# Kernel tuning notes

Hardware: AMD Instinct MI355X
Metric: run time of the kernel (lower is better)

The kernel has to match this reference:

```python
import jax, jax.numpy as jnp
import numpy as np

N = 100000   # nodes
E = 1600000  # edges
D = 128      # in_dim == hidden_dim
EL = 100000  # label edges for decode


def setup_inputs() -> dict:
    key = jax.random.key(0)
    k1, k2, k3, k4, k5 = jax.random.split(key, 5)
    x = jax.random.normal(k1, (N, D), dtype=jnp.float32)
    edge_index = jax.random.randint(k2, (2, E), 0, N, dtype=jnp.int64)
    edge_label_index = jax.random.randint(k3, (2, EL), 0, N, dtype=jnp.int64)
    # Glorot-ish init for GCN weights
    scale = 1.0 / np.sqrt(D)
    W1 = jax.random.normal(k4, (D, D), dtype=jnp.float32) * scale
    W2 = jax.random.normal(k5, (D, D), dtype=jnp.float32) * scale
    b1 = jnp.zeros((D,), dtype=jnp.float32)
    b2 = jnp.zeros((D,), dtype=jnp.float32)
    return {"x": x, "edge_index": edge_index, "edge_label_index": edge_label_index,
            "W1": W1, "b1": b1, "W2": W2, "b2": b2}


def gcn_conv(x, src, dst, W, b, num_nodes):
    # PyG GCNConv: add self-loops, symmetric D^-1/2 A D^-1/2 normalization
    loop = jnp.arange(num_nodes, dtype=src.dtype)
    s = jnp.concatenate([src, loop])
    d = jnp.concatenate([dst, loop])
    deg = jax.ops.segment_sum(jnp.ones(d.shape, dtype=x.dtype), d, num_segments=num_nodes)
    dinv = jnp.where(deg > 0, jax.lax.rsqrt(jnp.maximum(deg, 1.0)), 0.0)
    norm = dinv[s] * dinv[d]                      # [E+N]
    h = x @ W                                     # [N, H]
    msg = h[s] * norm[:, None]                    # gather + scale
    out = jax.ops.segment_sum(msg, d, num_segments=num_nodes)  # scatter-add
    return out + b


def reference(x, edge_index, edge_label_index, W1, b1, W2, b2):
    src, dst = edge_index[0], edge_index[1]
    z = jax.nn.relu(gcn_conv(x, src, dst, W1, b1, N))
    z = jax.nn.relu(gcn_conv(z, src, dst, W2, b2, N))
    # decode: edge-wise dot product
    s, d = edge_label_index[0], edge_label_index[1]
    return jnp.sum(z[s] * z[d], axis=-1)          # [EL]
```

## Files before the change

### kernel.cpp

```cpp
#include <hip/hip_runtime.h>
#include <hip/hip_bf16.h>
#include <hip/hip_fp16.h>


typedef _Float16 half8 __attribute__((ext_vector_type(8)));
typedef float floatx4 __attribute__((ext_vector_type(4)));

#define BK_SHIFT 8
#define BSC_EDGES 2048
#define SLAB_CAP 5120
#define WPAD 136

__global__ __launch_bounds__(128) void k_wprep(const float* __restrict__ W1,
                                               const float* __restrict__ W2,
                                               _Float16* __restrict__ WT1,
                                               _Float16* __restrict__ WT2,
                                               int* __restrict__ bfill) {
    int b = blockIdx.x;
    const float* W = (b < 128) ? W1 : W2;
    _Float16* WT = (b < 128) ? WT1 : WT2;
    int k = b & 127;
    int c = threadIdx.x;
    WT[c * 128 + k] = (_Float16)W[k * 128 + c];
    if (b < 4) bfill[b * 128 + c] = 0;
}

__global__ __launch_bounds__(256) void k_bscatter(const int* __restrict__ src,
                                                  const int* __restrict__ dst,
                                                  int* __restrict__ bfill,
                                                  int2* __restrict__ pairs,
                                                  int E, int nbk) {
    __shared__ int lcnt[1024];
    __shared__ int delta[1024];
    __shared__ int ssum[256];
    __shared__ int2 stage[BSC_EDGES];
    int tid = threadIdx.x;
    int e0 = blockIdx.x * BSC_EDGES;
    int nloc = E - e0; if (nloc > BSC_EDGES) nloc = BSC_EDGES;

    for (int b = tid; b < nbk; b += 256) lcnt[b] = 0;
    __syncthreads();

    int d[BSC_EDGES / 256], s[BSC_EDGES / 256];
#pragma unroll
    for (int k = 0; k < BSC_EDGES / 256; ++k) {
        int e = e0 + k * 256 + tid;
        if (e < E) {
            d[k] = dst[e];
            s[k] = src[e];
            atomicAdd(&lcnt[d[k] >> BK_SHIFT], 1);
        } else d[k] = -1;
    }
    __syncthreads();

    const int gpb = (nbk + 255) >> 8;
    int c[4], mysum = 0;
    for (int t = 0; t < gpb; ++t) {
        int b = tid * gpb + t;
        c[t] = (b < nbk) ? lcnt[b] : 0;
        mysum += c[t];
    }
    ssum[tid] = mysum;
    __syncthreads();
    for (int off = 1; off < 256; off <<= 1) {
        int t = (tid >= off) ? ssum[tid - off] : 0;
        __syncthreads();
        ssum[tid] += t;
        __syncthreads();
    }
    int base = ssum[tid] - mysum;
    for (int t = 0; t < gpb; ++t) {
        int b = tid * gpb + t;
        if (b < nbk) {
            int g = c[t] ? atomicAdd(&bfill[b], c[t]) : 0;
            delta[b] = b * SLAB_CAP + g - base;
            lcnt[b] = base;
            base += c[t];
        }
    }
    __syncthreads();

#pragma unroll
    for (int k = 0; k < BSC_EDGES / 256; ++k) {
        if (d[k] >= 0) {
            int b = d[k] >> BK_SHIFT;
            int lp = atomicAdd(&lcnt[b], 1);
            int2 p; p.x = s[k]; p.y = d[k];
            stage[lp] = p;
        }
    }
    __syncthreads();

    for (int j = tid; j < nloc; j += 256) {
        int2 p = stage[j];
        pairs[delta[p.y >> BK_SHIFT] + j] = p;
    }
}

template <typename AT>
__global__ __launch_bounds__(256) void k_csr_gemm(const int2* __restrict__ pairs,
                                                  const int* __restrict__ bfill,
                                                  int* __restrict__ row_start,
                                                  int* __restrict__ cnt,
                                                  float* __restrict__ dinv,
                                                  int* __restrict__ srcs,
                                                  const AT* __restrict__ X,
                                                  const _Float16* __restrict__ WT,
                                                  _Float16* __restrict__ G,
                                                  int n, int nbk) {
    __shared__ __align__(16) char smem[128 * WPAD * 2];
    int tid = threadIdx.x;

    if ((int)blockIdx.x < nbk) {
        int* lcnt = (int*)smem;
        int* lpos = lcnt + 256;
        int b = blockIdx.x;
        lcnt[tid] = 0;
        __syncthreads();
        int beg = b * SLAB_CAP, end = beg + bfill[b];
        for (int i = beg + tid; i < end; i += 256)
            atomicAdd(&lcnt[pairs[i].y & 255], 1);
        __syncthreads();
        int c = lcnt[tid];
        lpos[tid] = c;
        __syncthreads();
        for (int off = 1; off < 256; off <<= 1) {
            int t = (tid >= off) ? lpos[tid - off] : 0;
            __syncthreads();
            lpos[tid] += t;
            __syncthreads();
        }
        int rs = beg + lpos[tid] - c;
        int v = (b << BK_SHIFT) + tid;
        if (v < n) {
            row_start[v] = rs;
            cnt[v] = c;
            dinv[v] = rsqrtf((float)c + 1.0f);
        }
        __syncthreads();
        lpos[tid] = rs;
        __syncthreads();
        for (int i = beg + tid; i < end; i += 256) {
            int2 p = pairs[i];
            int loc = atomicAdd(&lpos[p.y & 255], 1);
            srcs[loc] = p.x;
        }
        return;
    }

    _Float16* Wl = (_Float16*)smem;
    {
        const half8* w8 = (const half8*)WT;
#pragma unroll
        for (int i = 0; i < 8; ++i) {
            int idx = i * 256 + tid;
            int r = idx >> 4, cc = idx & 15;
            *(half8*)(Wl + r * WPAD + cc * 8) = w8[idx];
        }
    }
    __syncthreads();

    auto loadA = [](const AT* p) -> half8 {
        if constexpr (sizeof(AT) == 4) {
            const float4* f = (const float4*)p;
            float4 f0 = f[0], f1 = f[1];
            half8 a;
            a[0] = (_Float16)f0.x; a[1] = (_Float16)f0.y;
            a[2] = (_Float16)f0.z; a[3] = (_Float16)f0.w;
            a[4] = (_Float16)f1.x; a[5] = (_Float16)f1.y;
            a[6] = (_Float16)f1.z; a[7] = (_Float16)f1.w;
            return a;
        } else {
            return *(const half8*)p;
        }
    };

    int bid = blockIdx.x - nbk;
    int wave = tid >> 6, lane = tid & 63;
    int q = lane >> 4, ln = lane & 15;
    int m0 = bid * 128 + wave * 32;
    int mA0 = m0 + ln;      if (mA0 >= n) mA0 = n - 1;
    int mA1 = m0 + 16 + ln; if (mA1 >= n) mA1 = n - 1;
    const AT* xr0 = X + (size_t)mA0 * 128;
    const AT* xr1 = X + (size_t)mA1 * 128;

    floatx4 acc[2][8];
#pragma unroll
    for (int p = 0; p < 2; ++p)
#pragma unroll
        for (int t = 0; t < 8; ++t) acc[p][t] = (floatx4){0.f, 0.f, 0.f, 0.f};

#pragma unroll
    for (int kc = 0; kc < 128; kc += 32) {
        half8 a0 = loadA(xr0 + kc + q * 8);
        half8 a1 = loadA(xr1 + kc + q * 8);
#pragma unroll
        for (int t = 0; t < 8; ++t) {
            half8 b = *(const half8*)(Wl + (size_t)(t * 16 + ln) * WPAD + kc + q * 8);
            acc[0][t] = __builtin_amdgcn_mfma_f32_16x16x32_f16(a0, b, acc[0][t], 0, 0, 0);
            acc[1][t] = __builtin_amdgcn_mfma_f32_16x16x32_f16(a1, b, acc[1][t], 0, 0, 0);
        }
    }

#pragma unroll
    for (int p = 0; p < 2; ++p) {
#pragma unroll
        for (int r = 0; r < 4; ++r) {
            int row = m0 + p * 16 + q * 4 + r;
            if (row < n) {
                _Float16* grow = G + (size_t)row * 128 + ln;
#pragma unroll
                for (int t = 0; t < 8; ++t)
                    grow[t * 16] = (_Float16)acc[p][t][r];
            }
        }
    }
}

template <typename AT>
__global__ __launch_bounds__(256) void k_gemm_mfma(const AT* __restrict__ X,
                                                   const _Float16* __restrict__ WT,
                                                   _Float16* __restrict__ G, int n) {
    __shared__ _Float16 Wl[128 * WPAD];
    int tid = threadIdx.x;
    {
        const half8* w8 = (const half8*)WT;
#pragma unroll
        for (int i = 0; i < 8; ++i) {
            int idx = i * 256 + tid;
            int r = idx >> 4, cc = idx & 15;
            *(half8*)(Wl + r * WPAD + cc * 8) = w8[idx];
        }
    }
    __syncthreads();

    auto loadA = [](const AT* p) -> half8 {
        if constexpr (sizeof(AT) == 4) {
            const float4* f = (const float4*)p;
            float4 f0 = f[0], f1 = f[1];
            half8 a;
            a[0] = (_Float16)f0.x; a[1] = (_Float16)f0.y;
            a[2] = (_Float16)f0.z; a[3] = (_Float16)f0.w;
            a[4] = (_Float16)f1.x; a[5] = (_Float16)f1.y;
            a[6] = (_Float16)f1.z; a[7] = (_Float16)f1.w;
            return a;
        } else {
            return *(const half8*)p;
        }
    };

    int wave = tid >> 6, lane = tid & 63;
    int q = lane >> 4, ln = lane & 15;
    int m0 = blockIdx.x * 128 + wave * 32;
    int mA0 = m0 + ln;      if (mA0 >= n) mA0 = n - 1;
    int mA1 = m0 + 16 + ln; if (mA1 >= n) mA1 = n - 1;
    const AT* xr0 = X + (size_t)mA0 * 128;
    const AT* xr1 = X + (size_t)mA1 * 128;

    floatx4 acc[2][8];
#pragma unroll
    for (int p = 0; p < 2; ++p)
#pragma unroll
        for (int t = 0; t < 8; ++t) acc[p][t] = (floatx4){0.f, 0.f, 0.f, 0.f};

#pragma unroll
    for (int kc = 0; kc < 128; kc += 32) {
        half8 a0 = loadA(xr0 + kc + q * 8);
        half8 a1 = loadA(xr1 + kc + q * 8);
#pragma unroll
        for (int t = 0; t < 8; ++t) {
            half8 b = *(const half8*)(Wl + (size_t)(t * 16 + ln) * WPAD + kc + q * 8);
            acc[0][t] = __builtin_amdgcn_mfma_f32_16x16x32_f16(a0, b, acc[0][t], 0, 0, 0);
            acc[1][t] = __builtin_amdgcn_mfma_f32_16x16x32_f16(a1, b, acc[1][t], 0, 0, 0);
        }
    }

#pragma unroll
    for (int p = 0; p < 2; ++p) {
#pragma unroll
        for (int r = 0; r < 4; ++r) {
            int row = m0 + p * 16 + q * 4 + r;
            if (row < n) {
                _Float16* grow = G + (size_t)row * 128 + ln;
#pragma unroll
                for (int t = 0; t < 8; ++t)
                    grow[t * 16] = (_Float16)acc[p][t][r];
            }
        }
    }
}

__global__ __launch_bounds__(256) void k_gather_relu(const _Float16* __restrict__ G,
                                                     const int* __restrict__ srcs,
                                                     const int* __restrict__ row_start,
                                                     const int* __restrict__ cnt,
                                                     const float* __restrict__ dinv,
                                                     const float* __restrict__ bias,
                                                     _Float16* __restrict__ Z, int n) {
    int v = blockIdx.x * 16 + (threadIdx.x >> 4);
    int lane = threadIdx.x & 15;
    if (v >= n) return;
    const half8* G8 = (const half8*)G;

    float dv = dinv[v];
    half8 self = G8[(size_t)v * 16 + lane];
    float acc[8], acc2[8];
#pragma unroll
    for (int j = 0; j < 8; ++j) { acc[j] = dv * (float)self[j]; acc2[j] = 0.f; }

    int beg = row_start[v], deg = cnt[v];
    int e = 0;
    for (; e + 3 < deg; e += 4) {
        int s0 = srcs[beg + e];
        int s1 = srcs[beg + e + 1];
        int s2 = srcs[beg + e + 2];
        int s3 = srcs[beg + e + 3];
        float d0 = dinv[s0];
        float d1 = dinv[s1];
        float d2 = dinv[s2];
        float d3 = dinv[s3];
        half8 t0 = G8[(size_t)s0 * 16 + lane];
        half8 t1 = G8[(size_t)s1 * 16 + lane];
        half8 t2 = G8[(size_t)s2 * 16 + lane];
        half8 t3 = G8[(size_t)s3 * 16 + lane];
#pragma unroll
        for (int j = 0; j < 8; ++j) {
            acc[j]  += d0 * (float)t0[j] + d1 * (float)t1[j];
            acc2[j] += d2 * (float)t2[j] + d3 * (float)t3[j];
        }
    }
    for (; e < deg; ++e) {
        int s0 = srcs[beg + e];
        float d0 = dinv[s0];
        half8 t0 = G8[(size_t)s0 * 16 + lane];
#pragma unroll
        for (int j = 0; j < 8; ++j) acc[j] += d0 * (float)t0[j];
    }

    const float4* b4 = (const float4*)bias;
    float4 bb0 = b4[lane * 2], bb1 = b4[lane * 2 + 1];
    float bf[8] = {bb0.x, bb0.y, bb0.z, bb0.w, bb1.x, bb1.y, bb1.z, bb1.w};
    half8 zo;
#pragma unroll
    for (int j = 0; j < 8; ++j) {
        float z = dv * (acc[j] + acc2[j]) + bf[j];
        zo[j] = (_Float16)fmaxf(z, 0.f);
    }
    ((half8*)Z)[(size_t)v * 16 + lane] = zo;
}

__global__ __launch_bounds__(256) void k_decode(const _Float16* __restrict__ Z,
                                                const int* __restrict__ eli,
                                                float* __restrict__ out, int el) {
    int sub = threadIdx.x >> 4, lane = threadIdx.x & 15;
    int e = blockIdx.x * 16 + sub;
    if (e >= el) return;
    int s = eli[e], d = eli[el + e];
    const half8* Z8 = (const half8*)Z;
    half8 a = Z8[(size_t)s * 16 + lane];
    half8 b = Z8[(size_t)d * 16 + lane];
    float dot = 0.f;
#pragma unroll
    for (int j = 0; j < 8; ++j) dot += (float)a[j] * (float)b[j];
#pragma unroll
    for (int off = 8; off; off >>= 1) dot += __shfl_down(dot, off, 16);
    if (lane == 0) out[e] = dot;
}

extern "C" void kernel_launch(void* const* d_in, const int* in_sizes, int n_in,
                              void* d_out, int out_size, void* d_ws, size_t ws_size,
                              hipStream_t stream) {
    const float* x  = (const float*)d_in[0];
    const int*  ei  = (const int*)d_in[1];
    const int*  eli = (const int*)d_in[2];
    const float* W1 = (const float*)d_in[3];
    const float* b1 = (const float*)d_in[4];
    const float* W2 = (const float*)d_in[5];
    const float* b2 = (const float*)d_in[6];
    float* out = (float*)d_out;

    const int N  = in_sizes[0] / 128;
    const int E  = in_sizes[1] / 2;
    const int EL = in_sizes[2] / 2;
    const int* src = ei;
    const int* dst = ei + E;
    const int NBK = (N + 255) >> BK_SHIFT;
    const int GB  = (N + 127) / 128;

    char* ws = (char*)d_ws;
    size_t off = 0;
    auto alloc = [&](size_t bytes) -> void* {
        void* p = ws + off;
        off += bytes;
        off = (off + 255) & ~(size_t)255;
        return p;
    };
    int*       cnt       = (int*)alloc((size_t)N * 4);
    int*       row_start = (int*)alloc((size_t)N * 4);
    float*     dinv      = (float*)alloc((size_t)N * 4);
    int*       bfill     = (int*)alloc(4096);
    _Float16*  WT1       = (_Float16*)alloc(128 * 128 * 2);
    _Float16*  WT2       = (_Float16*)alloc(128 * 128 * 2);
    int*       srcs      = (int*)alloc((size_t)NBK * SLAB_CAP * 4);
    int2*      pairs     = (int2*)alloc((size_t)NBK * SLAB_CAP * 8);
    _Float16*  buf0      = (_Float16*)alloc((size_t)N * 128 * 2);
    _Float16*  buf1      = (_Float16*)alloc((size_t)N * 128 * 2);

    k_wprep<<<256, 128, 0, stream>>>(W1, W2, WT1, WT2, bfill);

    k_bscatter<<<(E + BSC_EDGES - 1) / BSC_EDGES, 256, 0, stream>>>(src, dst, bfill, pairs, E, NBK);

    k_csr_gemm<float><<<NBK + GB, 256, 0, stream>>>(pairs, bfill, row_start, cnt, dinv,
                                                    srcs, x, WT1, buf0, N, NBK);

    k_gather_relu<<<(N + 15) / 16, 256, 0, stream>>>(buf0, srcs, row_start, cnt, dinv, b1, buf1, N);
    k_gemm_mfma<_Float16><<<GB, 256, 0, stream>>>(buf1, WT2, buf0, N);
    k_gather_relu<<<(N + 15) / 16, 256, 0, stream>>>(buf0, srcs, row_start, cnt, dinv, b2, buf1, N);
    k_decode<<<(EL + 15) / 16, 256, 0, stream>>>(buf1, eli, out, EL);
}
```

Before: 307.6 us.

## Replace global-atomic slab scatter with per-block bins and offset table

The edge bucketing step no longer reserves space in per-bucket slabs with global atomics. Each edge block now writes its locally sorted edges, packed as (src<<8 | dst&255) in 4 bytes, into its own contiguous bin and records per-bucket offsets in a table P. Each CSR-building block then walks all bins to gather its bucket's edges into shared memory before counting and placing them. The weight transpose is folded into the binning kernel, which removes one launch and the bfill reset. In exchange, each CSR block reads roughly 782 offset pairs with short serial copy loops. Packing src<<8 also limits node ids to below 2^23.

```diff
diff --git a/kernel.cpp b/kernel.cpp
--- a/kernel.cpp
+++ b/kernel.cpp
@@ -11,30 +11,31 @@
 #define SLAB_CAP 5120
 #define WPAD 136
 
-__global__ __launch_bounds__(128) void k_wprep(const float* __restrict__ W1,
-                                               const float* __restrict__ W2,
-                                               _Float16* __restrict__ WT1,
-                                               _Float16* __restrict__ WT2,
-                                               int* __restrict__ bfill) {
-    int b = blockIdx.x;
-    const float* W = (b < 128) ? W1 : W2;
-    _Float16* WT = (b < 128) ? WT1 : WT2;
-    int k = b & 127;
-    int c = threadIdx.x;
-    WT[c * 128 + k] = (_Float16)W[k * 128 + c];
-    if (b < 4) bfill[b * 128 + c] = 0;
-}
-
-__global__ __launch_bounds__(256) void k_bscatter(const int* __restrict__ src,
-                                                  const int* __restrict__ dst,
-                                                  int* __restrict__ bfill,
-                                                  int2* __restrict__ pairs,
-                                                  int E, int nbk) {
+__global__ __launch_bounds__(256) void k_bin(const int* __restrict__ src,
+                                             const int* __restrict__ dst,
+                                             int* __restrict__ bins,
+                                             int* __restrict__ P,
+                                             int E, int nbk, int nbin,
+                                             const float* __restrict__ W1,
+                                             const float* __restrict__ W2,
+                                             _Float16* __restrict__ WT1,
+                                             _Float16* __restrict__ WT2) {
+    int tid = threadIdx.x;
+    if ((int)blockIdx.x >= nbin) {
+        int b2 = blockIdx.x - nbin;
+        if (tid < 128) {
+            const float* W = (b2 < 128) ? W1 : W2;
+            _Float16* WT = (b2 < 128) ? WT1 : WT2;
+            int k = b2 & 127;
+            WT[tid * 128 + k] = (_Float16)W[k * 128 + tid];
+        }
+        return;
+    }
+
     __shared__ int lcnt[1024];
     __shared__ int delta[1024];
     __shared__ int ssum[256];
-    __shared__ int2 stage[BSC_EDGES];
-    int tid = threadIdx.x;
+    __shared__ int stage[BSC_EDGES];
     int e0 = blockIdx.x * BSC_EDGES;
     int nloc = E - e0; if (nloc > BSC_EDGES) nloc = BSC_EDGES;
 
@@ -72,8 +73,7 @@
     for (int t = 0; t < gpb; ++t) {
         int b = tid * gpb + t;
         if (b < nbk) {
-            int g = c[t] ? atomicAdd(&bfill[b], c[t]) : 0;
-            delta[b] = b * SLAB_CAP + g - base;
+            delta[b] = base;
             lcnt[b] = base;
             base += c[t];
         }
@@ -85,21 +85,22 @@
         if (d[k] >= 0) {
             int b = d[k] >> BK_SHIFT;
             int lp = atomicAdd(&lcnt[b], 1);
-            int2 p; p.x = s[k]; p.y = d[k];
-            stage[lp] = p;
-        }
-    }
-    __syncthreads();
-
-    for (int j = tid; j < nloc; j += 256) {
-        int2 p = stage[j];
-        pairs[delta[p.y >> BK_SHIFT] + j] = p;
-    }
+            stage[lp] = (s[k] << 8) | (d[k] & 255);
+        }
+    }
+    __syncthreads();
+
+    int* bb = bins + (size_t)blockIdx.x * BSC_EDGES;
+    for (int j = tid; j < nloc; j += 256) bb[j] = stage[j];
+    int prow = nbk + 1;
+    int* pp = P + (size_t)blockIdx.x * prow;
+    for (int b = tid; b <= nbk; b += 256)
+        pp[b] = (b < nbk) ? delta[b] : nloc;
 }
 
 template <typename AT>
-__global__ __launch_bounds__(256) void k_csr_gemm(const int2* __restrict__ pairs,
-                                                  const int* __restrict__ bfill,
+__global__ __launch_bounds__(256) void k_csr_gemm(const int* __restrict__ bins,
+                                                  const int* __restrict__ P,
                                                   int* __restrict__ row_start,
                                                   int* __restrict__ cnt,
                                                   float* __restrict__ dinv,
@@ -107,19 +108,35 @@
                                                   const AT* __restrict__ X,
                                                   const _Float16* __restrict__ WT,
                                                   _Float16* __restrict__ G,
-                                                  int n, int nbk) {
+                                                  int n, int nbk, int nbin) {
     __shared__ __align__(16) char smem[128 * WPAD * 2];
     int tid = threadIdx.x;
 
     if ((int)blockIdx.x < nbk) {
-        int* lcnt = (int*)smem;
-        int* lpos = lcnt + 256;
+        int* stage = (int*)smem;
+        int* lcnt  = (int*)(smem + 20480);
+        int* lpos  = (int*)(smem + 21504);
+        int* curs  = (int*)(smem + 22528);
         int b = blockIdx.x;
+        int prow = nbk + 1;
+        if (tid == 0) *curs = 0;
+        __syncthreads();
+        for (int seg = tid; seg < nbin; seg += 256) {
+            const int* pp = P + (size_t)seg * prow + b;
+            int p0 = pp[0], p1 = pp[1];
+            int len = p1 - p0;
+            if (len > 0) {
+                int off = atomicAdd(curs, len);
+                const int* sp = bins + (size_t)seg * BSC_EDGES + p0;
+                for (int i = 0; i < len; ++i) stage[off + i] = sp[i];
+            }
+        }
+        __syncthreads();
+        int tot = *curs;
         lcnt[tid] = 0;
         __syncthreads();
-        int beg = b * SLAB_CAP, end = beg + bfill[b];
-        for (int i = beg + tid; i < end; i += 256)
-            atomicAdd(&lcnt[pairs[i].y & 255], 1);
+        for (int i = tid; i < tot; i += 256)
+            atomicAdd(&lcnt[stage[i] & 255], 1);
         __syncthreads();
         int c = lcnt[tid];
         lpos[tid] = c;
@@ -130,7 +147,7 @@
             lpos[tid] += t;
             __syncthreads();
         }
-        int rs = beg + lpos[tid] - c;
+        int rs = b * SLAB_CAP + lpos[tid] - c;
         int v = (b << BK_SHIFT) + tid;
         if (v < n) {
             row_start[v] = rs;
@@ -140,10 +157,10 @@
         __syncthreads();
         lpos[tid] = rs;
         __syncthreads();
-        for (int i = beg + tid; i < end; i += 256) {
-            int2 p = pairs[i];
-            int loc = atomicAdd(&lpos[p.y & 255], 1);
-            srcs[loc] = p.x;
+        for (int i = tid; i < tot; i += 256) {
+            int p = stage[i];
+            int loc = atomicAdd(&lpos[p & 255], 1);
+            srcs[loc] = p >> 8;
         }
         return;
     }
@@ -384,8 +401,9 @@
     const int EL = in_sizes[2] / 2;
     const int* src = ei;
     const int* dst = ei + E;
-    const int NBK = (N + 255) >> BK_SHIFT;
-    const int GB  = (N + 127) / 128;
+    const int NBK  = (N + 255) >> BK_SHIFT;
+    const int NBIN = (E + BSC_EDGES - 1) / BSC_EDGES;
+    const int GB   = (N + 127) / 128;
 
     char* ws = (char*)d_ws;
     size_t off = 0;
@@ -398,20 +416,19 @@
     int*       cnt       = (int*)alloc((size_t)N * 4);
     int*       row_start = (int*)alloc((size_t)N * 4);
     float*     dinv      = (float*)alloc((size_t)N * 4);
-    int*       bfill     = (int*)alloc(4096);
     _Float16*  WT1       = (_Float16*)alloc(128 * 128 * 2);
     _Float16*  WT2       = (_Float16*)alloc(128 * 128 * 2);
     int*       srcs      = (int*)alloc((size_t)NBK * SLAB_CAP * 4);
-    int2*      pairs     = (int2*)alloc((size_t)NBK * SLAB_CAP * 8);
+    int*       bins      = (int*)alloc((size_t)NBIN * BSC_EDGES * 4);
+    int*       P         = (int*)alloc((size_t)NBIN * (NBK + 1) * 4);
     _Float16*  buf0      = (_Float16*)alloc((size_t)N * 128 * 2);
     _Float16*  buf1      = (_Float16*)alloc((size_t)N * 128 * 2);
 
-    k_wprep<<<256, 128, 0, stream>>>(W1, W2, WT1, WT2, bfill);
-
-    k_bscatter<<<(E + BSC_EDGES - 1) / BSC_EDGES, 256, 0, stream>>>(src, dst, bfill, pairs, E, NBK);
-
-    k_csr_gemm<float><<<NBK + GB, 256, 0, stream>>>(pairs, bfill, row_start, cnt, dinv,
-                                                    srcs, x, WT1, buf0, N, NBK);
+    k_bin<<<NBIN + 256, 256, 0, stream>>>(src, dst, bins, P, E, NBK, NBIN,
+                                          W1, W2, WT1, WT2);
+
+    k_csr_gemm<float><<<NBK + GB, 256, 0, stream>>>(bins, P, row_start, cnt, dinv,
+                                                    srcs, x, WT1, buf0, N, NBK, NBIN);
 
     k_gather_relu<<<(N + 15) / 16, 256, 0, stream>>>(buf0, srcs, row_start, cnt, dinv, b1, buf1, N);
     k_gemm_mfma<_Float16><<<GB, 256, 0, stream>>>(buf1, WT2, buf0, N);
```

Result: faster. 277.9 us (-9.7%).
